# Optimization experiments

Measured on AMD Instinct MI355X. Metric: run time of the kernel, lower is better.

The kernel has to match this reference:

```python
import jax, jax.numpy as jnp
import numpy as np

B, L, F_DIM, H = 4, 384, 640, 128
K_COULOMB = 332.0
DIELECTRIC = 80.0
BN_EPS = 1e-5

# amino-acid charge table, index order 'ACDEFGHIKLMNPQRSTVWY'
_AA = 'ACDEFGHIKLMNPQRSTVWY'
_CHG = {'D': -1.0, 'E': -1.0, 'K': 1.0, 'R': 1.0, 'H': 0.1}
_TABLE = np.zeros((20, 3), dtype=np.float32)
for _i, _aa in enumerate(_AA):
    c = _CHG.get(_aa, 0.0)
    _TABLE[_i, 0 if c > 0 else (1 if c < 0 else 2)] = 1.0
CHG_TABLE = jnp.asarray(_TABLE)


def _conv1d(x, w, b, pad):
    # x: [N, Cin, L], w: [Cout, Cin, K]
    y = jax.lax.conv_general_dilated(x, w, (1,), [(pad, pad)],
                                     dimension_numbers=('NCH', 'OIH', 'NCH'))
    return y + b[None, :, None]


def setup_inputs() -> dict:
    key = jax.random.key(0)
    ks = jax.random.split(key, 32)
    s = 0.05

    def rn(k, shape):
        return (jax.random.normal(k, shape) * s).astype(jnp.float32)

    inp = {
        'features': jax.random.normal(ks[0], (B, L, F_DIM), dtype=jnp.float32),
        'seq_ids': jax.random.randint(ks[1], (B, L), 0, 20, dtype=jnp.int32),
        'structures': (jax.random.normal(ks[2], (B, L, 3)) * 10.0).astype(jnp.float32),
        # charge predictor: Linear(F,H) -> ReLU -> BN(H) -> Linear(H,H//2) -> ReLU -> Linear(H//2,3) -> Softmax
        'W1': rn(ks[3], (F_DIM, H)), 'b1': jnp.zeros((H,), jnp.float32),
        'gamma': jnp.ones((H,), jnp.float32), 'beta': jnp.zeros((H,), jnp.float32),
        'rmean': jnp.zeros((H,), jnp.float32), 'rvar': jnp.ones((H,), jnp.float32),
        'W2': rn(ks[4], (H, H // 2)), 'b2': jnp.zeros((H // 2,), jnp.float32),
        'W3': rn(ks[5], (H // 2, 3)), 'b3': jnp.zeros((3,), jnp.float32),
        # salt bridge detector: Linear(2F+1,H) -> ReLU -> Linear(H,64) -> ReLU -> Linear(64,1) -> Sigmoid
        'sW1': rn(ks[6], (2 * F_DIM + 1, H)), 'sb1': jnp.zeros((H,), jnp.float32),
        'sW2': rn(ks[7], (H, 64)), 'sb2': jnp.zeros((64,), jnp.float32),
        'sW3': rn(ks[8], (64, 1)), 'sb3': jnp.zeros((1,), jnp.float32),
        # potential calculator convs (OIH layout)
        'c1w': rn(ks[9], (16, 1, 5)), 'c1b': jnp.zeros((16,), jnp.float32),
        'c2w': rn(ks[10], (8, 16, 3)), 'c2b': jnp.zeros((8,), jnp.float32),
        'c3w': rn(ks[11], (1, 8, 3)), 'c3b': jnp.zeros((1,), jnp.float32),
    }
    return inp


def reference(features, seq_ids, structures,
              W1, b1, gamma, beta, rmean, rvar, W2, b2, W3, b3,
              sW1, sb1, sW2, sb2, sW3, sb3,
              c1w, c1b, c2w, c2b, c3w, c3b):
    b_, l_, f_ = features.shape

    # true charges from sequence (one-hot pos/neg/neutral)
    true_charges = CHG_TABLE[seq_ids]                               # [B,L,3]

    # --- charge predictor (BatchNorm in eval mode: running stats) ---
    x = features.reshape(-1, f_)
    h = jax.nn.relu(x @ W1 + b1)
    h = gamma * (h - rmean) / jnp.sqrt(rvar + BN_EPS) + beta
    h = jax.nn.relu(h @ W2 + b2)
    pc = jax.nn.softmax(h @ W3 + b3, axis=-1).reshape(b_, l_, 3)    # [B,L,3]

    net_charge = pc[:, :, 0:1] - pc[:, :, 1:2]                      # [B,L,1]

    # --- electrostatic potential: 1D conv stack on [B,1,L] ---
    p = net_charge.transpose(0, 2, 1)                               # [B,1,L]
    p = jax.nn.relu(_conv1d(p, c1w, c1b, 2))
    p = jax.nn.relu(_conv1d(p, c2w, c2b, 1))
    p = _conv1d(p, c3w, c3b, 1)
    potential = p.transpose(0, 2, 1)                                # [B,L,1]

    # --- pairwise distances ---
    diff = structures[:, :, None, :] - structures[:, None, :, :]    # [B,L,L,3]
    D = jnp.sqrt(jnp.sum(diff * diff, axis=-1) + 1e-12)             # [B,L,L]

    # --- salt bridges: vectorized edge-MLP over all (pos i, neg j) pairs ---
    pos = pc[:, :, 0] > pc[:, :, 2]                                 # [B,L]
    neg = pc[:, :, 1] > pc[:, :, 2]                                 # [B,L]
    a, bb, d = sW1[:f_], sW1[f_:2 * f_], sW1[2 * f_]                # split cat([fi,fj,dist]) @ sW1
    fi = features @ a                                               # [B,L,H]
    fj = features @ bb                                              # [B,L,H]
    hid = jax.nn.relu(fi[:, :, None, :] + fj[:, None, :, :] + D[..., None] * d + sb1)  # [B,L,L,H]
    hid2 = jax.nn.relu(hid @ sW2 + sb2)                             # [B,L,L,64]
    prob = jax.nn.sigmoid((hid2 @ sW3 + sb3)[..., 0])               # [B,L,L]
    q = pos[:, :, None] & neg[:, None, :] & (D < 4.0) & (prob > 0.5)
    salt_bridge_masks = (q | q.transpose(0, 2, 1)).astype(jnp.float32)  # [B,L,L]

    # --- Coulomb energy with distance-dependent dielectric ---
    # dielectric = eps * D / 4 -> e_ij = k * q_i q_j / (eps/4 * D^2)
    qc = pc[:, :, 0] - pc[:, :, 1]                                  # [B,L]
    valid = (D < 15.0) & (D > 0.0)
    triu = jnp.triu(jnp.ones((l_, l_), bool), k=1)[None]
    D_safe = jnp.where(valid, D, 1.0)
    e_ij = K_COULOMB * qc[:, :, None] * qc[:, None, :] / ((DIELECTRIC / 4.0) * D_safe * D_safe)
    energy = jnp.sum(jnp.where(valid & triu, e_ij, 0.0), axis=(1, 2))  # [B]

    return (pc, true_charges, net_charge, potential, salt_bridge_masks, energy)
```

## Files before the change

### kernel.cpp

```cpp
#include <hip/hip_runtime.h>

#define LSEQ 384
#define NROWS 1536
#define FDIM 640
#define HDIM 128
#define PART 196608

#define WS_FI   0
#define WS_FJ   393216
#define WS_QC   786432
#define WS_FLAG 787968

#define OUT_PC    0
#define OUT_TC    4608
#define OUT_NET   9216
#define OUT_POT   10752
#define OUT_MASK  12288
#define OUT_EN    602112

__global__ __launch_bounds__(256) void k1(const float* __restrict__ X,
                                          const float* __restrict__ W1,
                                          const float* __restrict__ sW1,
                                          const float* __restrict__ b1,
                                          const float* __restrict__ gam,
                                          const float* __restrict__ bet,
                                          const float* __restrict__ rmean,
                                          const float* __restrict__ rvar,
                                          const float* __restrict__ W2,
                                          const float* __restrict__ b2,
                                          const float* __restrict__ W3,
                                          const float* __restrict__ b3,
                                          const int* __restrict__ seq,
                                          float* __restrict__ out,
                                          float* __restrict__ ws) {
    __shared__ char smem[27648];
    const int t = threadIdx.x;
    const int blk = blockIdx.x;

    if (blk == 0 && t < 4) out[OUT_EN + t] = 0.0f;

    if (blk < 96) {
        float* As = (float*)smem;
        float* Bs = (float*)(smem + 2304);
        float* hs = (float*)(smem + 18688);
        const int m0 = blk * 16;
        const int tx = (t & 31) * 4;
        const int ty = (t >> 5) * 2;
        float acc[2][4] = {};
        for (int kk = 0; kk < FDIM; kk += 32) {
            if (t < 128) {
                int a_r = t >> 3, a_c = (t & 7) * 4;
                float4 av = *(const float4*)&X[(m0 + a_r) * FDIM + kk + a_c];
                As[(a_c + 0) * 18 + a_r] = av.x;
                As[(a_c + 1) * 18 + a_r] = av.y;
                As[(a_c + 2) * 18 + a_r] = av.z;
                As[(a_c + 3) * 18 + a_r] = av.w;
            }
#pragma unroll
            for (int q = 0; q < 4; q++) {
                int idx = t + 256 * q;
                int r = idx >> 5, c4 = (idx & 31) * 4;
                *(float4*)&Bs[r * 128 + c4] = *(const float4*)&W1[(kk + r) * HDIM + c4];
            }
            __syncthreads();
#pragma unroll
            for (int k = 0; k < 32; k++) {
                float2 a = *(const float2*)&As[k * 18 + ty];
                float4 b = *(const float4*)&Bs[k * 128 + tx];
                acc[0][0] = fmaf(a.x, b.x, acc[0][0]);
                acc[0][1] = fmaf(a.x, b.y, acc[0][1]);
                acc[0][2] = fmaf(a.x, b.z, acc[0][2]);
                acc[0][3] = fmaf(a.x, b.w, acc[0][3]);
                acc[1][0] = fmaf(a.y, b.x, acc[1][0]);
                acc[1][1] = fmaf(a.y, b.y, acc[1][1]);
                acc[1][2] = fmaf(a.y, b.z, acc[1][2]);
                acc[1][3] = fmaf(a.y, b.w, acc[1][3]);
            }
            __syncthreads();
        }
        {
            float4 b1v = *(const float4*)&b1[tx];
            float4 g4  = *(const float4*)&gam[tx];
            float4 be4 = *(const float4*)&bet[tx];
            float4 rm4 = *(const float4*)&rmean[tx];
            float4 rv4 = *(const float4*)&rvar[tx];
            float rs0 = 1.0f / sqrtf(rv4.x + 1e-5f);
            float rs1 = 1.0f / sqrtf(rv4.y + 1e-5f);
            float rs2 = 1.0f / sqrtf(rv4.z + 1e-5f);
            float rs3 = 1.0f / sqrtf(rv4.w + 1e-5f);
#pragma unroll
            for (int r = 0; r < 2; r++) {
                float v0 = g4.x * (fmaxf(acc[r][0] + b1v.x, 0.0f) - rm4.x) * rs0 + be4.x;
                float v1 = g4.y * (fmaxf(acc[r][1] + b1v.y, 0.0f) - rm4.y) * rs1 + be4.y;
                float v2 = g4.z * (fmaxf(acc[r][2] + b1v.z, 0.0f) - rm4.z) * rs2 + be4.z;
                float v3 = g4.w * (fmaxf(acc[r][3] + b1v.w, 0.0f) - rm4.w) * rs3 + be4.w;
                *(float4*)&hs[(ty + r) * 132 + tx] = make_float4(v0, v1, v2, v3);
            }
        }
        __syncthreads();
        const int w = t >> 6, lane = t & 63;
        float h0r[4], h1r[4], acc2[4];
#pragma unroll
        for (int r = 0; r < 4; r++) {
            h0r[r] = hs[(w * 4 + r) * 132 + lane];
            h1r[r] = hs[(w * 4 + r) * 132 + 64 + lane];
            acc2[r] = b2[lane];
        }
#pragma unroll
        for (int cc = 0; cc < 64; cc++) {
            float wv0 = W2[cc * 64 + lane];
            float wv1 = W2[(cc + 64) * 64 + lane];
#pragma unroll
            for (int r = 0; r < 4; r++) {
                float hv0 = __uint_as_float(__builtin_amdgcn_readlane(__float_as_uint(h0r[r]), cc));
                float hv1 = __uint_as_float(__builtin_amdgcn_readlane(__float_as_uint(h1r[r]), cc));
                acc2[r] = fmaf(hv0, wv0, acc2[r]);
                acc2[r] = fmaf(hv1, wv1, acc2[r]);
            }
        }
        float w30 = W3[lane * 3 + 0], w31 = W3[lane * 3 + 1], w32 = W3[lane * 3 + 2];
#pragma unroll
        for (int r = 0; r < 4; r++) {
            float h2 = fmaxf(acc2[r], 0.0f);
            float x0 = h2 * w30, x1 = h2 * w31, x2 = h2 * w32;
#pragma unroll
            for (int o = 32; o > 0; o >>= 1) {
                x0 += __shfl_xor(x0, o, 64);
                x1 += __shfl_xor(x1, o, 64);
                x2 += __shfl_xor(x2, o, 64);
            }
            if (lane == 0) {
                int row = m0 + w * 4 + r;
                float l0 = x0 + b3[0], l1 = x1 + b3[1], l2 = x2 + b3[2];
                float m = fmaxf(l0, fmaxf(l1, l2));
                float e0 = expf(l0 - m), e1 = expf(l1 - m), e2 = expf(l2 - m);
                float s = e0 + e1 + e2;
                float pc0 = e0 / s, pc1 = e1 / s, pc2 = e2 / s;
                out[OUT_PC + row * 3 + 0] = pc0;
                out[OUT_PC + row * 3 + 1] = pc1;
                out[OUT_PC + row * 3 + 2] = pc2;
                float net = pc0 - pc1;
                out[OUT_NET + row] = net;
                ws[WS_QC + row] = net;
                ((int*)(ws + WS_FLAG))[row] = (pc0 > pc2 ? 1 : 0) | (pc1 > pc2 ? 2 : 0);
                int sid = seq[row];
                float c0 = (sid == 6 || sid == 8 || sid == 14) ? 1.0f : 0.0f;
                float c1 = (sid == 2 || sid == 3) ? 1.0f : 0.0f;
                out[OUT_TC + row * 3 + 0] = c0;
                out[OUT_TC + row * 3 + 1] = c1;
                out[OUT_TC + row * 3 + 2] = (c0 == 0.0f && c1 == 0.0f) ? 1.0f : 0.0f;
            }
        }
    } else {
        float* As = (float*)smem;
        float* Bs = (float*)(smem + 4352);
        const int bi = blk - 96;
        const int kz = bi & 1, half = (bi >> 1) & 1, mat = (bi >> 2) & 1, mt = bi >> 3;
        const int m0 = mt * 32, n0 = half * 64;
        const float* W = sW1 + mat * 640 * 128;
        float* O = ws + (mat == 0 ? WS_FI : WS_FJ) + kz * PART;
        const int a_r = t >> 3, a_c = (t & 7) * 4;
        const int b_r = t >> 4, b_c = (t & 15) * 4;
        const int tx = (t & 15) * 4, ty = (t >> 4) * 2;
        float acc[2][4] = {};
        const int k0 = kz * 320;
        for (int kk = k0; kk < k0 + 320; kk += 32) {
            float4 av = *(const float4*)&X[(m0 + a_r) * FDIM + kk + a_c];
            As[(a_c + 0) * 34 + a_r] = av.x;
            As[(a_c + 1) * 34 + a_r] = av.y;
            As[(a_c + 2) * 34 + a_r] = av.z;
            As[(a_c + 3) * 34 + a_r] = av.w;
            *(float4*)&Bs[b_r * 64 + b_c]        = *(const float4*)&W[(kk + b_r) * HDIM + n0 + b_c];
            *(float4*)&Bs[(b_r + 16) * 64 + b_c] = *(const float4*)&W[(kk + b_r + 16) * HDIM + n0 + b_c];
            __syncthreads();
#pragma unroll
            for (int k = 0; k < 32; k++) {
                float2 a = *(const float2*)&As[k * 34 + ty];
                float4 b = *(const float4*)&Bs[k * 64 + tx];
                acc[0][0] = fmaf(a.x, b.x, acc[0][0]);
                acc[0][1] = fmaf(a.x, b.y, acc[0][1]);
                acc[0][2] = fmaf(a.x, b.z, acc[0][2]);
                acc[0][3] = fmaf(a.x, b.w, acc[0][3]);
                acc[1][0] = fmaf(a.y, b.x, acc[1][0]);
                acc[1][1] = fmaf(a.y, b.y, acc[1][1]);
                acc[1][2] = fmaf(a.y, b.z, acc[1][2]);
                acc[1][3] = fmaf(a.y, b.w, acc[1][3]);
            }
            __syncthreads();
        }
#pragma unroll
        for (int r = 0; r < 2; r++) {
            float4 v = make_float4(acc[r][0], acc[r][1], acc[r][2], acc[r][3]);
            *(float4*)&O[(m0 + ty + r) * HDIM + n0 + tx] = v;
        }
    }
}

__device__ __forceinline__ float mlp_eval(const float* __restrict__ fiA, const float* __restrict__ fiB,
                                          const float* __restrict__ fjA, const float* __restrict__ fjB,
                                          int gi, int gj, float D,
                                          float dv0, float dv1, float sb0, float sb1v,
                                          float b2v, float w3l, const float* w2s, int lane) {
    float fi0 = fiA[gi * 128 + lane]      + fiB[gi * 128 + lane];
    float fi1 = fiA[gi * 128 + 64 + lane] + fiB[gi * 128 + 64 + lane];
    float fj0 = fjA[gj * 128 + lane]      + fjB[gj * 128 + lane];
    float fj1 = fjA[gj * 128 + 64 + lane] + fjB[gj * 128 + 64 + lane];
    float h0 = fmaxf(fi0 + fj0 + D * dv0 + sb0, 0.0f);
    float h1 = fmaxf(fi1 + fj1 + D * dv1 + sb1v, 0.0f);
    float a0 = 0.0f, a1 = 0.0f;
#pragma unroll
    for (int cc = 0; cc < 64; cc++) {
        float hv0 = __uint_as_float(__builtin_amdgcn_readlane(__float_as_uint(h0), cc));
        float hv1 = __uint_as_float(__builtin_amdgcn_readlane(__float_as_uint(h1), cc));
        a0 = fmaf(hv0, w2s[cc * 64 + lane], a0);
        a1 = fmaf(hv1, w2s[(cc + 64) * 64 + lane], a1);
    }
    float x = fmaxf(a0 + a1 + b2v, 0.0f) * w3l;
#pragma unroll
    for (int o = 32; o > 0; o >>= 1) x += __shfl_xor(x, o, 64);
    return x;
}

__global__ __launch_bounds__(256) void k2(const float* __restrict__ S,
                                          const float* __restrict__ ws,
                                          const float* __restrict__ sW1,
                                          const float* __restrict__ sb1,
                                          const float* __restrict__ sW2,
                                          const float* __restrict__ sb2,
                                          const float* __restrict__ sW3,
                                          const float* __restrict__ sb3,
                                          const float* __restrict__ c1w, const float* __restrict__ c1b,
                                          const float* __restrict__ c2w, const float* __restrict__ c2b,
                                          const float* __restrict__ c3w, const float* __restrict__ c3b,
                                          float* __restrict__ out) {
    __shared__ char smem[40960];
    const int t = threadIdx.x;
    const int bi = blockIdx.x;

    if (bi < 4) {
        float* p0 = (float*)smem;
        float* p1 = p0 + 388;
        float* p2 = p1 + 16 * 386;
        const int b = bi;
        for (int j = t; j < LSEQ; j += 256) p0[j + 2] = out[OUT_NET + b * LSEQ + j];
        if (t < 2) { p0[t] = 0.0f; p0[LSEQ + 2 + t] = 0.0f; }
        if (t < 16) { p1[t * 386] = 0.0f; p1[t * 386 + 385] = 0.0f; }
        if (t < 8)  { p2[t * 386] = 0.0f; p2[t * 386 + 385] = 0.0f; }
        __syncthreads();
        for (int pos = t; pos < LSEQ; pos += 256) {
#pragma unroll
            for (int o = 0; o < 16; o++) {
                float acc = c1b[o];
#pragma unroll
                for (int k = 0; k < 5; k++) acc = fmaf(p0[pos + k], c1w[o * 5 + k], acc);
                p1[o * 386 + pos + 1] = fmaxf(acc, 0.0f);
            }
        }
        __syncthreads();
        for (int pos = t; pos < LSEQ; pos += 256) {
#pragma unroll
            for (int o = 0; o < 8; o++) {
                float acc = c2b[o];
                for (int i = 0; i < 16; i++)
#pragma unroll
                    for (int k = 0; k < 3; k++)
                        acc = fmaf(p1[i * 386 + pos + k], c2w[(o * 16 + i) * 3 + k], acc);
                p2[o * 386 + pos + 1] = fmaxf(acc, 0.0f);
            }
        }
        __syncthreads();
        for (int pos = t; pos < LSEQ; pos += 256) {
            float acc = c3b[0];
            for (int i = 0; i < 8; i++)
#pragma unroll
                for (int k = 0; k < 3; k++)
                    acc = fmaf(p2[i * 386 + pos + k], c3w[i * 3 + k], acc);
            out[OUT_POT + b * LSEQ + pos] = acc;
        }
        return;
    }

    float* sx = (float*)smem;
    float* sy = sx + 384;
    float* sz = sy + 384;
    float* sq = sz + 384;
    unsigned int* clist = (unsigned int*)(sz + 768);
    unsigned char* sf = (unsigned char*)(smem + 7680);
    float* red = (float*)(smem + 8064);
    int* cntL = (int*)(smem + 8080);
    float* w2s = (float*)(smem + 8192);

    const float* qc = ws + WS_QC;
    const int* flags = (const int*)(ws + WS_FLAG);
    const float* fiA = ws + WS_FI;
    const float* fiB = ws + WS_FI + PART;
    const float* fjA = ws + WS_FJ;
    const float* fjB = ws + WS_FJ + PART;

    const int row = bi - 4;
    const int b = row / LSEQ;
    const int i = row - b * LSEQ;

    for (int j = t; j < LSEQ; j += 256) {
        int g = b * LSEQ + j;
        sx[j] = S[g * 3 + 0];
        sy[j] = S[g * 3 + 1];
        sz[j] = S[g * 3 + 2];
        sq[j] = qc[g];
        sf[j] = (unsigned char)flags[g];
    }
    if (t == 0) *cntL = 0;
    __syncthreads();

    const float six = sx[i], siy = sy[i], siz = sz[i], qi = sq[i];
    const int fli = sf[i];
    const bool posi = (fli & 1) != 0, negi = (fli & 2) != 0;
    const int lane = t & 63, w = t >> 6;
    float esum = 0.0f;
    float* mrow = out + OUT_MASK + (long)row * LSEQ;

    for (int j = t; j < LSEQ; j += 256) {
        float dx = __fsub_rn(six, sx[j]);
        float dy = __fsub_rn(siy, sy[j]);
        float dz = __fsub_rn(siz, sz[j]);
        float d2 = __fadd_rn(__fadd_rn(__fmul_rn(dx, dx), __fmul_rn(dy, dy)), __fmul_rn(dz, dz));
        d2 = __fadd_rn(d2, 1e-12f);
        float D = __fsqrt_rn(d2);
        mrow[j] = 0.0f;
        if (j > i && D < 15.0f && D > 0.0f) {
            float num = __fmul_rn(__fmul_rn(332.0f, qi), sq[j]);
            float den = __fmul_rn(__fmul_rn(20.0f, D), D);
            esum += __fdiv_rn(num, den);
        }
        int flj = sf[j];
        bool near = (D < 4.0f);
        bool need1 = near && posi && ((flj & 2) != 0);
        bool need2 = near && negi && ((flj & 1) != 0);
        if (need1 || need2) {
            int p = atomicAdd(cntL, 1);
            clist[p] = (unsigned int)j | (need1 ? 512u : 0u) | (need2 ? 1024u : 0u);
        }
    }
#pragma unroll
    for (int o = 32; o > 0; o >>= 1) esum += __shfl_xor(esum, o, 64);
    if (lane == 0) red[w] = esum;
    __syncthreads();
    if (t == 0) {
        float s = red[0] + red[1] + red[2] + red[3];
        atomicAdd(&out[OUT_EN + b], s);
    }

    int nc = *cntL;
    if (nc == 0) return;

    for (int idx = t; idx < 2048; idx += 256)
        ((float4*)w2s)[idx] = ((const float4*)sW2)[idx];
    const float* dvec = sW1 + 1280 * 128;
    const float dv0 = dvec[lane], dv1 = dvec[lane + 64];
    const float sb0 = sb1[lane], sb1v = sb1[lane + 64];
    const float w3l = sW3[lane];
    const float b2v = sb2[lane];
    const float b3v = sb3[0];
    __syncthreads();

    for (int c = w; c < nc; c += 4) {
        unsigned int e = clist[c];
        int j = (int)(e & 511u);
        bool need1 = (e & 512u) != 0, need2 = (e & 1024u) != 0;
        float dx = __fsub_rn(six, sx[j]);
        float dy = __fsub_rn(siy, sy[j]);
        float dz = __fsub_rn(siz, sz[j]);
        float d2 = __fadd_rn(__fadd_rn(__fmul_rn(dx, dx), __fmul_rn(dy, dy)), __fmul_rn(dz, dz));
        d2 = __fadd_rn(d2, 1e-12f);
        float D = __fsqrt_rn(d2);
        int gi = row, gj = b * LSEQ + j;
        bool hit = false;
        if (need1) {
            float x = mlp_eval(fiA, fiB, fjA, fjB, gi, gj, D, dv0, dv1, sb0, sb1v, b2v, w3l, w2s, lane);
            hit = (x + b3v) > 0.0f;
        }
        if (!hit && need2) {
            float x = mlp_eval(fiA, fiB, fjA, fjB, gj, gi, D, dv0, dv1, sb0, sb1v, b2v, w3l, w2s, lane);
            hit = (x + b3v) > 0.0f;
        }
        if (hit && lane == 0) mrow[j] = 1.0f;
    }
}

extern "C" void kernel_launch(void* const* d_in, const int* in_sizes, int n_in,
                              void* d_out, int out_size, void* d_ws, size_t ws_size,
                              hipStream_t stream) {
    const float* X     = (const float*)d_in[0];
    const int*   seq   = (const int*)d_in[1];
    const float* S     = (const float*)d_in[2];
    const float* W1    = (const float*)d_in[3];
    const float* b1    = (const float*)d_in[4];
    const float* gam   = (const float*)d_in[5];
    const float* bet   = (const float*)d_in[6];
    const float* rmean = (const float*)d_in[7];
    const float* rvar  = (const float*)d_in[8];
    const float* W2    = (const float*)d_in[9];
    const float* b2    = (const float*)d_in[10];
    const float* W3    = (const float*)d_in[11];
    const float* b3    = (const float*)d_in[12];
    const float* sW1   = (const float*)d_in[13];
    const float* sb1   = (const float*)d_in[14];
    const float* sW2   = (const float*)d_in[15];
    const float* sb2   = (const float*)d_in[16];
    const float* sW3   = (const float*)d_in[17];
    const float* sb3   = (const float*)d_in[18];
    const float* c1w   = (const float*)d_in[19];
    const float* c1b   = (const float*)d_in[20];
    const float* c2w   = (const float*)d_in[21];
    const float* c2b   = (const float*)d_in[22];
    const float* c3w   = (const float*)d_in[23];
    const float* c3b   = (const float*)d_in[24];

    float* out = (float*)d_out;
    float* ws  = (float*)d_ws;

    hipLaunchKernelGGL(k1, dim3(480), dim3(256), 0, stream,
                       X, W1, sW1, b1, gam, bet, rmean, rvar, W2, b2, W3, b3,
                       seq, out, ws);
    hipLaunchKernelGGL(k2, dim3(1540), dim3(256), 0, stream,
                       S, ws, sW1, sb1, sW2, sb2, sW3, sb3,
                       c1w, c1b, c2w, c2b, c3w, c3b, out);
}
```

Measured before the change: 171.5 us.

## Split first-stage GEMMs into uniform split-K kernel plus per-row reduction kernel

Replaces the heterogeneous k1 kernel, where 96 blocks each ran a full 640-deep GEMM plus an MLP tail while the other blocks ran half-K GEMMs, with a uniform 48x6x4 grid using 4-way split-K and double-buffered shared-memory tiles. A new k_row kernel sums the partials, applies BN and the small MLP, and writes pre-reduced fi/fj, so the pairwise kernel reads one array instead of two. The goal is to remove load imbalance from the long-running charge-predictor blocks and to overlap global loads with compute. The cost is an extra launch and extra workspace traffic for the partial sums.

```diff
diff --git a/kernel.cpp b/kernel.cpp
--- a/kernel.cpp
+++ b/kernel.cpp
@@ -6,10 +6,13 @@
 #define HDIM 128
 #define PART 196608
 
-#define WS_FI   0
-#define WS_FJ   393216
-#define WS_QC   786432
-#define WS_FLAG 787968
+#define WS_H1P 0
+#define WS_FIP (4*PART)
+#define WS_FJP (8*PART)
+#define WS_FI  (12*PART)
+#define WS_FJ  (13*PART)
+#define WS_QC  (14*PART)
+#define WS_FLAG (WS_QC + NROWS)
 
 #define OUT_PC    0
 #define OUT_TC    4608
@@ -18,193 +21,176 @@
 #define OUT_MASK  12288
 #define OUT_EN    602112
 
-__global__ __launch_bounds__(256) void k1(const float* __restrict__ X,
-                                          const float* __restrict__ W1,
-                                          const float* __restrict__ sW1,
-                                          const float* __restrict__ b1,
-                                          const float* __restrict__ gam,
-                                          const float* __restrict__ bet,
-                                          const float* __restrict__ rmean,
-                                          const float* __restrict__ rvar,
-                                          const float* __restrict__ W2,
-                                          const float* __restrict__ b2,
-                                          const float* __restrict__ W3,
-                                          const float* __restrict__ b3,
-                                          const int* __restrict__ seq,
-                                          float* __restrict__ out,
-                                          float* __restrict__ ws) {
-    __shared__ char smem[27648];
+__global__ __launch_bounds__(256) void k_gemm(const float* __restrict__ X,
+                                              const float* __restrict__ W1,
+                                              const float* __restrict__ sW1,
+                                              float* __restrict__ ws,
+                                              float* __restrict__ out) {
+    __shared__ float As[2 * 32 * 34];
+    __shared__ float Bs[2 * 32 * 64];
     const int t = threadIdx.x;
-    const int blk = blockIdx.x;
-
-    if (blk == 0 && t < 4) out[OUT_EN + t] = 0.0f;
-
-    if (blk < 96) {
-        float* As = (float*)smem;
-        float* Bs = (float*)(smem + 2304);
-        float* hs = (float*)(smem + 18688);
-        const int m0 = blk * 16;
-        const int tx = (t & 31) * 4;
-        const int ty = (t >> 5) * 2;
-        float acc[2][4] = {};
-        for (int kk = 0; kk < FDIM; kk += 32) {
-            if (t < 128) {
-                int a_r = t >> 3, a_c = (t & 7) * 4;
-                float4 av = *(const float4*)&X[(m0 + a_r) * FDIM + kk + a_c];
-                As[(a_c + 0) * 18 + a_r] = av.x;
-                As[(a_c + 1) * 18 + a_r] = av.y;
-                As[(a_c + 2) * 18 + a_r] = av.z;
-                As[(a_c + 3) * 18 + a_r] = av.w;
-            }
-#pragma unroll
-            for (int q = 0; q < 4; q++) {
-                int idx = t + 256 * q;
-                int r = idx >> 5, c4 = (idx & 31) * 4;
-                *(float4*)&Bs[r * 128 + c4] = *(const float4*)&W1[(kk + r) * HDIM + c4];
-            }
+    if (blockIdx.x == 0 && blockIdx.y == 0 && blockIdx.z == 0 && t < 4)
+        out[OUT_EN + t] = 0.0f;
+
+    const int m0 = blockIdx.x * 32;
+    const int gy = blockIdx.y, kz = blockIdx.z;
+    const int mat = gy >> 1, half = gy & 1, n0 = half * 64;
+    const float* W = (mat == 0) ? W1 : (mat == 1 ? sW1 : sW1 + 640 * 128);
+    float* O = ws + (mat == 0 ? WS_H1P : (mat == 1 ? WS_FIP : WS_FJP)) + kz * PART;
+
+    const int a_r = t >> 3, a_c = (t & 7) * 4;
+    const int b_r = t >> 4, b_c = (t & 15) * 4;
+    const int tx = (t & 15) * 4, ty = (t >> 4) * 2;
+    const int k0 = kz * 160;
+
+    float acc[2][4] = {};
+
+    float4 av  = *(const float4*)&X[(m0 + a_r) * FDIM + k0 + a_c];
+    float4 bv0 = *(const float4*)&W[(k0 + b_r) * HDIM + n0 + b_c];
+    float4 bv1 = *(const float4*)&W[(k0 + b_r + 16) * HDIM + n0 + b_c];
+    As[(a_c + 0) * 34 + a_r] = av.x;
+    As[(a_c + 1) * 34 + a_r] = av.y;
+    As[(a_c + 2) * 34 + a_r] = av.z;
+    As[(a_c + 3) * 34 + a_r] = av.w;
+    *(float4*)&Bs[b_r * 64 + b_c]        = bv0;
+    *(float4*)&Bs[(b_r + 16) * 64 + b_c] = bv1;
+    __syncthreads();
+
+    for (int it = 0; it < 5; it++) {
+        const int buf = it & 1;
+        if (it < 4) {
+            const int kk = k0 + (it + 1) * 32;
+            av  = *(const float4*)&X[(m0 + a_r) * FDIM + kk + a_c];
+            bv0 = *(const float4*)&W[(kk + b_r) * HDIM + n0 + b_c];
+            bv1 = *(const float4*)&W[(kk + b_r + 16) * HDIM + n0 + b_c];
+        }
+        const float* Ab = As + buf * 1088;
+        const float* Bb = Bs + buf * 2048;
+#pragma unroll
+        for (int k = 0; k < 32; k++) {
+            float2 a = *(const float2*)&Ab[k * 34 + ty];
+            float4 b = *(const float4*)&Bb[k * 64 + tx];
+            acc[0][0] = fmaf(a.x, b.x, acc[0][0]);
+            acc[0][1] = fmaf(a.x, b.y, acc[0][1]);
+            acc[0][2] = fmaf(a.x, b.z, acc[0][2]);
+            acc[0][3] = fmaf(a.x, b.w, acc[0][3]);
+            acc[1][0] = fmaf(a.y, b.x, acc[1][0]);
+            acc[1][1] = fmaf(a.y, b.y, acc[1][1]);
+            acc[1][2] = fmaf(a.y, b.z, acc[1][2]);
+            acc[1][3] = fmaf(a.y, b.w, acc[1][3]);
+        }
+        if (it < 4) {
+            float* Aw = As + (buf ^ 1) * 1088;
+            float* Bw = Bs + (buf ^ 1) * 2048;
+            Aw[(a_c + 0) * 34 + a_r] = av.x;
+            Aw[(a_c + 1) * 34 + a_r] = av.y;
+            Aw[(a_c + 2) * 34 + a_r] = av.z;
+            Aw[(a_c + 3) * 34 + a_r] = av.w;
+            *(float4*)&Bw[b_r * 64 + b_c]        = bv0;
+            *(float4*)&Bw[(b_r + 16) * 64 + b_c] = bv1;
             __syncthreads();
-#pragma unroll
-            for (int k = 0; k < 32; k++) {
-                float2 a = *(const float2*)&As[k * 18 + ty];
-                float4 b = *(const float4*)&Bs[k * 128 + tx];
-                acc[0][0] = fmaf(a.x, b.x, acc[0][0]);
-                acc[0][1] = fmaf(a.x, b.y, acc[0][1]);
-                acc[0][2] = fmaf(a.x, b.z, acc[0][2]);
-                acc[0][3] = fmaf(a.x, b.w, acc[0][3]);
-                acc[1][0] = fmaf(a.y, b.x, acc[1][0]);
-                acc[1][1] = fmaf(a.y, b.y, acc[1][1]);
-                acc[1][2] = fmaf(a.y, b.z, acc[1][2]);
-                acc[1][3] = fmaf(a.y, b.w, acc[1][3]);
-            }
-            __syncthreads();
-        }
-        {
-            float4 b1v = *(const float4*)&b1[tx];
-            float4 g4  = *(const float4*)&gam[tx];
-            float4 be4 = *(const float4*)&bet[tx];
-            float4 rm4 = *(const float4*)&rmean[tx];
-            float4 rv4 = *(const float4*)&rvar[tx];
-            float rs0 = 1.0f / sqrtf(rv4.x + 1e-5f);
-            float rs1 = 1.0f / sqrtf(rv4.y + 1e-5f);
-            float rs2 = 1.0f / sqrtf(rv4.z + 1e-5f);
-            float rs3 = 1.0f / sqrtf(rv4.w + 1e-5f);
-#pragma unroll
-            for (int r = 0; r < 2; r++) {
-                float v0 = g4.x * (fmaxf(acc[r][0] + b1v.x, 0.0f) - rm4.x) * rs0 + be4.x;
-                float v1 = g4.y * (fmaxf(acc[r][1] + b1v.y, 0.0f) - rm4.y) * rs1 + be4.y;
-                float v2 = g4.z * (fmaxf(acc[r][2] + b1v.z, 0.0f) - rm4.z) * rs2 + be4.z;
-                float v3 = g4.w * (fmaxf(acc[r][3] + b1v.w, 0.0f) - rm4.w) * rs3 + be4.w;
-                *(float4*)&hs[(ty + r) * 132 + tx] = make_float4(v0, v1, v2, v3);
-            }
-        }
-        __syncthreads();
-        const int w = t >> 6, lane = t & 63;
-        float h0r[4], h1r[4], acc2[4];
-#pragma unroll
-        for (int r = 0; r < 4; r++) {
-            h0r[r] = hs[(w * 4 + r) * 132 + lane];
-            h1r[r] = hs[(w * 4 + r) * 132 + 64 + lane];
-            acc2[r] = b2[lane];
-        }
-#pragma unroll
-        for (int cc = 0; cc < 64; cc++) {
-            float wv0 = W2[cc * 64 + lane];
-            float wv1 = W2[(cc + 64) * 64 + lane];
-#pragma unroll
-            for (int r = 0; r < 4; r++) {
-                float hv0 = __uint_as_float(__builtin_amdgcn_readlane(__float_as_uint(h0r[r]), cc));
-                float hv1 = __uint_as_float(__builtin_amdgcn_readlane(__float_as_uint(h1r[r]), cc));
-                acc2[r] = fmaf(hv0, wv0, acc2[r]);
-                acc2[r] = fmaf(hv1, wv1, acc2[r]);
-            }
-        }
-        float w30 = W3[lane * 3 + 0], w31 = W3[lane * 3 + 1], w32 = W3[lane * 3 + 2];
-#pragma unroll
-        for (int r = 0; r < 4; r++) {
-            float h2 = fmaxf(acc2[r], 0.0f);
-            float x0 = h2 * w30, x1 = h2 * w31, x2 = h2 * w32;
-#pragma unroll
-            for (int o = 32; o > 0; o >>= 1) {
-                x0 += __shfl_xor(x0, o, 64);
-                x1 += __shfl_xor(x1, o, 64);
-                x2 += __shfl_xor(x2, o, 64);
-            }
-            if (lane == 0) {
-                int row = m0 + w * 4 + r;
-                float l0 = x0 + b3[0], l1 = x1 + b3[1], l2 = x2 + b3[2];
-                float m = fmaxf(l0, fmaxf(l1, l2));
-                float e0 = expf(l0 - m), e1 = expf(l1 - m), e2 = expf(l2 - m);
-                float s = e0 + e1 + e2;
-                float pc0 = e0 / s, pc1 = e1 / s, pc2 = e2 / s;
-                out[OUT_PC + row * 3 + 0] = pc0;
-                out[OUT_PC + row * 3 + 1] = pc1;
-                out[OUT_PC + row * 3 + 2] = pc2;
-                float net = pc0 - pc1;
-                out[OUT_NET + row] = net;
-                ws[WS_QC + row] = net;
-                ((int*)(ws + WS_FLAG))[row] = (pc0 > pc2 ? 1 : 0) | (pc1 > pc2 ? 2 : 0);
-                int sid = seq[row];
-                float c0 = (sid == 6 || sid == 8 || sid == 14) ? 1.0f : 0.0f;
-                float c1 = (sid == 2 || sid == 3) ? 1.0f : 0.0f;
-                out[OUT_TC + row * 3 + 0] = c0;
-                out[OUT_TC + row * 3 + 1] = c1;
-                out[OUT_TC + row * 3 + 2] = (c0 == 0.0f && c1 == 0.0f) ? 1.0f : 0.0f;
-            }
-        }
-    } else {
-        float* As = (float*)smem;
-        float* Bs = (float*)(smem + 4352);
-        const int bi = blk - 96;
-        const int kz = bi & 1, half = (bi >> 1) & 1, mat = (bi >> 2) & 1, mt = bi >> 3;
-        const int m0 = mt * 32, n0 = half * 64;
-        const float* W = sW1 + mat * 640 * 128;
-        float* O = ws + (mat == 0 ? WS_FI : WS_FJ) + kz * PART;
-        const int a_r = t >> 3, a_c = (t & 7) * 4;
-        const int b_r = t >> 4, b_c = (t & 15) * 4;
-        const int tx = (t & 15) * 4, ty = (t >> 4) * 2;
-        float acc[2][4] = {};
-        const int k0 = kz * 320;
-        for (int kk = k0; kk < k0 + 320; kk += 32) {
-            float4 av = *(const float4*)&X[(m0 + a_r) * FDIM + kk + a_c];
-            As[(a_c + 0) * 34 + a_r] = av.x;
-            As[(a_c + 1) * 34 + a_r] = av.y;
-            As[(a_c + 2) * 34 + a_r] = av.z;
-            As[(a_c + 3) * 34 + a_r] = av.w;
-            *(float4*)&Bs[b_r * 64 + b_c]        = *(const float4*)&W[(kk + b_r) * HDIM + n0 + b_c];
-            *(float4*)&Bs[(b_r + 16) * 64 + b_c] = *(const float4*)&W[(kk + b_r + 16) * HDIM + n0 + b_c];
-            __syncthreads();
-#pragma unroll
-            for (int k = 0; k < 32; k++) {
-                float2 a = *(const float2*)&As[k * 34 + ty];
-                float4 b = *(const float4*)&Bs[k * 64 + tx];
-                acc[0][0] = fmaf(a.x, b.x, acc[0][0]);
-                acc[0][1] = fmaf(a.x, b.y, acc[0][1]);
-                acc[0][2] = fmaf(a.x, b.z, acc[0][2]);
-                acc[0][3] = fmaf(a.x, b.w, acc[0][3]);
-                acc[1][0] = fmaf(a.y, b.x, acc[1][0]);
-                acc[1][1] = fmaf(a.y, b.y, acc[1][1]);
-                acc[1][2] = fmaf(a.y, b.z, acc[1][2]);
-                acc[1][3] = fmaf(a.y, b.w, acc[1][3]);
-            }
-            __syncthreads();
-        }
-#pragma unroll
-        for (int r = 0; r < 2; r++) {
-            float4 v = make_float4(acc[r][0], acc[r][1], acc[r][2], acc[r][3]);
-            *(float4*)&O[(m0 + ty + r) * HDIM + n0 + tx] = v;
-        }
+        }
+    }
+#pragma unroll
+    for (int r = 0; r < 2; r++) {
+        float4 v = make_float4(acc[r][0], acc[r][1], acc[r][2], acc[r][3]);
+        *(float4*)&O[(m0 + ty + r) * HDIM + n0 + tx] = v;
     }
 }
 
-__device__ __forceinline__ float mlp_eval(const float* __restrict__ fiA, const float* __restrict__ fiB,
-                                          const float* __restrict__ fjA, const float* __restrict__ fjB,
+__global__ __launch_bounds__(256) void k_row(float* __restrict__ ws,
+                                             const float* __restrict__ b1,
+                                             const float* __restrict__ gam,
+                                             const float* __restrict__ bet,
+                                             const float* __restrict__ rmean,
+                                             const float* __restrict__ rvar,
+                                             const float* __restrict__ W2,
+                                             const float* __restrict__ b2,
+                                             const float* __restrict__ W3,
+                                             const float* __restrict__ b3,
+                                             const int* __restrict__ seq,
+                                             float* __restrict__ out) {
+    const int t = threadIdx.x, w = t >> 6, lane = t & 63;
+    const int row = blockIdx.x * 4 + w;
+    const long base = (long)row * 128;
+    const float* h1p = ws + WS_H1P;
+    const float* fip = ws + WS_FIP;
+    const float* fjp = ws + WS_FJP;
+
+    {
+        float fi0 = fip[base + lane] + fip[PART + base + lane]
+                  + fip[2 * PART + base + lane] + fip[3 * PART + base + lane];
+        float fi1 = fip[base + 64 + lane] + fip[PART + base + 64 + lane]
+                  + fip[2 * PART + base + 64 + lane] + fip[3 * PART + base + 64 + lane];
+        float fj0 = fjp[base + lane] + fjp[PART + base + lane]
+                  + fjp[2 * PART + base + lane] + fjp[3 * PART + base + lane];
+        float fj1 = fjp[base + 64 + lane] + fjp[PART + base + 64 + lane]
+                  + fjp[2 * PART + base + 64 + lane] + fjp[3 * PART + base + 64 + lane];
+        ws[WS_FI + base + lane]      = fi0;
+        ws[WS_FI + base + 64 + lane] = fi1;
+        ws[WS_FJ + base + lane]      = fj0;
+        ws[WS_FJ + base + 64 + lane] = fj1;
+    }
+
+    float h0 = h1p[base + lane] + h1p[PART + base + lane]
+             + h1p[2 * PART + base + lane] + h1p[3 * PART + base + lane];
+    float h1 = h1p[base + 64 + lane] + h1p[PART + base + 64 + lane]
+             + h1p[2 * PART + base + 64 + lane] + h1p[3 * PART + base + 64 + lane];
+    h0 = fmaxf(h0 + b1[lane], 0.0f);
+    h1 = fmaxf(h1 + b1[64 + lane], 0.0f);
+    h0 = gam[lane]      * (h0 - rmean[lane])      / sqrtf(rvar[lane] + 1e-5f)      + bet[lane];
+    h1 = gam[64 + lane] * (h1 - rmean[64 + lane]) / sqrtf(rvar[64 + lane] + 1e-5f) + bet[64 + lane];
+
+    float acc = b2[lane];
+#pragma unroll
+    for (int cc = 0; cc < 64; cc++) {
+        float wv0 = W2[cc * 64 + lane];
+        float wv1 = W2[(cc + 64) * 64 + lane];
+        float hv0 = __uint_as_float(__builtin_amdgcn_readlane(__float_as_uint(h0), cc));
+        float hv1 = __uint_as_float(__builtin_amdgcn_readlane(__float_as_uint(h1), cc));
+        acc = fmaf(hv0, wv0, acc);
+        acc = fmaf(hv1, wv1, acc);
+    }
+    float h2 = fmaxf(acc, 0.0f);
+    float x0 = h2 * W3[lane * 3 + 0];
+    float x1 = h2 * W3[lane * 3 + 1];
+    float x2 = h2 * W3[lane * 3 + 2];
+#pragma unroll
+    for (int o = 32; o > 0; o >>= 1) {
+        x0 += __shfl_xor(x0, o, 64);
+        x1 += __shfl_xor(x1, o, 64);
+        x2 += __shfl_xor(x2, o, 64);
+    }
+    if (lane == 0) {
+        float l0 = x0 + b3[0], l1 = x1 + b3[1], l2 = x2 + b3[2];
+        float m = fmaxf(l0, fmaxf(l1, l2));
+        float e0 = expf(l0 - m), e1 = expf(l1 - m), e2 = expf(l2 - m);
+        float s = e0 + e1 + e2;
+        float pc0 = e0 / s, pc1 = e1 / s, pc2 = e2 / s;
+        out[OUT_PC + row * 3 + 0] = pc0;
+        out[OUT_PC + row * 3 + 1] = pc1;
+        out[OUT_PC + row * 3 + 2] = pc2;
+        float net = pc0 - pc1;
+        out[OUT_NET + row] = net;
+        ws[WS_QC + row] = net;
+        ((int*)(ws + WS_FLAG))[row] = (pc0 > pc2 ? 1 : 0) | (pc1 > pc2 ? 2 : 0);
+        int sid = seq[row];
+        float c0 = (sid == 6 || sid == 8 || sid == 14) ? 1.0f : 0.0f;
+        float c1 = (sid == 2 || sid == 3) ? 1.0f : 0.0f;
+        out[OUT_TC + row * 3 + 0] = c0;
+        out[OUT_TC + row * 3 + 1] = c1;
+        out[OUT_TC + row * 3 + 2] = (c0 == 0.0f && c1 == 0.0f) ? 1.0f : 0.0f;
+    }
+}
+
+__device__ __forceinline__ float mlp_eval(const float* __restrict__ fi, const float* __restrict__ fj,
                                           int gi, int gj, float D,
                                           float dv0, float dv1, float sb0, float sb1v,
                                           float b2v, float w3l, const float* w2s, int lane) {
-    float fi0 = fiA[gi * 128 + lane]      + fiB[gi * 128 + lane];
-    float fi1 = fiA[gi * 128 + 64 + lane] + fiB[gi * 128 + 64 + lane];
-    float fj0 = fjA[gj * 128 + lane]      + fjB[gj * 128 + lane];
-    float fj1 = fjA[gj * 128 + 64 + lane] + fjB[gj * 128 + 64 + lane];
+    float fi0 = fi[(long)gi * 128 + lane];
+    float fi1 = fi[(long)gi * 128 + 64 + lane];
+    float fj0 = fj[(long)gj * 128 + lane];
+    float fj1 = fj[(long)gj * 128 + 64 + lane];
     float h0 = fmaxf(fi0 + fj0 + D * dv0 + sb0, 0.0f);
     float h1 = fmaxf(fi1 + fj1 + D * dv1 + sb1v, 0.0f);
     float a0 = 0.0f, a1 = 0.0f;
@@ -292,10 +278,8 @@
 
     const float* qc = ws + WS_QC;
     const int* flags = (const int*)(ws + WS_FLAG);
-    const float* fiA = ws + WS_FI;
-    const float* fiB = ws + WS_FI + PART;
-    const float* fjA = ws + WS_FJ;
-    const float* fjB = ws + WS_FJ + PART;
+    const float* fi = ws + WS_FI;
+    const float* fj = ws + WS_FJ;
 
     const int row = bi - 4;
     const int b = row / LSEQ;
@@ -376,11 +360,11 @@
         int gi = row, gj = b * LSEQ + j;
         bool hit = false;
         if (need1) {
-            float x = mlp_eval(fiA, fiB, fjA, fjB, gi, gj, D, dv0, dv1, sb0, sb1v, b2v, w3l, w2s, lane);
+            float x = mlp_eval(fi, fj, gi, gj, D, dv0, dv1, sb0, sb1v, b2v, w3l, w2s, lane);
             hit = (x + b3v) > 0.0f;
         }
         if (!hit && need2) {
-            float x = mlp_eval(fiA, fiB, fjA, fjB, gj, gi, D, dv0, dv1, sb0, sb1v, b2v, w3l, w2s, lane);
+            float x = mlp_eval(fi, fj, gj, gi, D, dv0, dv1, sb0, sb1v, b2v, w3l, w2s, lane);
             hit = (x + b3v) > 0.0f;
         }
         if (hit && lane == 0) mrow[j] = 1.0f;
@@ -419,9 +403,9 @@
     float* out = (float*)d_out;
     float* ws  = (float*)d_ws;
 
-    hipLaunchKernelGGL(k1, dim3(480), dim3(256), 0, stream,
-                       X, W1, sW1, b1, gam, bet, rmean, rvar, W2, b2, W3, b3,
-                       seq, out, ws);
+    hipLaunchKernelGGL(k_gemm, dim3(48, 6, 4), dim3(256), 0, stream, X, W1, sW1, ws, out);
+    hipLaunchKernelGGL(k_row, dim3(384), dim3(256), 0, stream,
+                       ws, b1, gam, bet, rmean, rvar, W2, b2, W3, b3, seq, out);
     hipLaunchKernelGGL(k2, dim3(1540), dim3(256), 0, stream,
                        S, ws, sW1, sb1, sW2, sb2, sW3, sb3,
                        c1w, c1b, c2w, c2b, c3w, c3b, out);
```

Result: faster. 155.8 us (-9.2%).
